# Performance work log

Hardware: AMD Instinct MI355X
Metric: run time of the kernel (lower is better)

Reference implementation:

```python
import jax, jax.numpy as jnp
import numpy as np

P = 2.0            # power-mean exponent (init kwarg p)
NUM_NODES = 1_000_000
D_FEAT = 128
NUM_GRAPHS = 4096


def setup_inputs() -> dict:
    key = jax.random.key(0)
    kx, kb = jax.random.split(key)
    x = jax.random.normal(kx, (NUM_NODES, D_FEAT), dtype=jnp.float32)
    batch = jnp.sort(jax.random.randint(kb, (NUM_NODES,), 0, NUM_GRAPHS, dtype=jnp.int64))
    return {"x": x, "batch": batch}


def reference(x, batch):
    # x: [N, D] node features; batch: [N] sorted graph ids in [0, NUM_GRAPHS)
    xp = x ** P                                                   # elementwise pow
    seg_sum = jax.ops.segment_sum(xp, batch, num_segments=NUM_GRAPHS)  # [G, D]
    counts = jax.ops.segment_sum(jnp.ones((x.shape[0],), dtype=x.dtype), batch,
                                 num_segments=NUM_GRAPHS)         # [G]
    # scatter_mean semantics: empty segments yield 0 (clamp count to avoid 0/0)
    mean = seg_sum / jnp.maximum(counts, 1.0)[:, None]            # [G, D]
    return mean ** (1.0 / P)
```

## Files before the change

### kernel.cpp

```cpp
#include <hip/hip_runtime.h>
#include <math.h>


#define D_FEAT 128
#define DV 32
#define SWEEP_GRID 2048
#define CHUNK 64

typedef float f32x4 __attribute__((ext_vector_type(4)));

__device__ __forceinline__ void nt_load4x(
    const f32x4* p0, const f32x4* p1, const f32x4* p2, const f32x4* p3,
    f32x4& v0, f32x4& v1, f32x4& v2, f32x4& v3)
{
    asm volatile(
        "global_load_dwordx4 %0, %4, off sc0 sc1 nt\n\t"
        "global_load_dwordx4 %1, %5, off sc0 sc1 nt\n\t"
        "global_load_dwordx4 %2, %6, off sc0 sc1 nt\n\t"
        "global_load_dwordx4 %3, %7, off sc0 sc1 nt\n\t"
        "s_waitcnt vmcnt(0)"
        : "=&v"(v0), "=&v"(v1), "=&v"(v2), "=&v"(v3)
        : "v"(p0), "v"(p1), "v"(p2), "v"(p3));
}

__device__ __forceinline__ f32x4 nt_load1(const f32x4* p)
{
    f32x4 v;
    asm volatile(
        "global_load_dwordx4 %0, %1, off sc0 sc1 nt\n\t"
        "s_waitcnt vmcnt(0)"
        : "=&v"(v) : "v"(p));
    return v;
}

__global__ __launch_bounds__(256) void seg_offsets_kernel(
    const int* __restrict__ batch, int* __restrict__ off, int N, int G)
{
    int i = blockIdx.x * blockDim.x + threadIdx.x;
    if (i >= N) return;
    int cur = batch[i];
    if (i == 0) {
        for (int g = 0; g <= cur; ++g) off[g] = 0;
    } else {
        int prev = batch[i - 1];
        for (int g = prev + 1; g <= cur; ++g) off[g] = i;
    }
    if (i == N - 1) {
        for (int g = cur + 1; g <= G; ++g) off[g] = N;
    }
}

__global__ __launch_bounds__(256) void zero_out_kernel(f32x4* __restrict__ out4, int n4)
{
    int i = blockIdx.x * 256 + threadIdx.x;
    if (i < n4) out4[i] = (f32x4)0.f;
}

__global__ __launch_bounds__(256) void global_powermean_pooling_44126493999223_kernel(
    const f32x4* __restrict__ x4,
    const int*   __restrict__ batch,
    const int*   __restrict__ off,
    float*       __restrict__ out,
    int N)
{
    const int tid  = threadIdx.x;
    const int fg   = tid & 31;
    const int lane = tid >> 5;

    __shared__ f32x4 red[256];

    const int nchunks = (N + CHUNK - 1) / CHUNK;
    for (int c = blockIdx.x; c < nchunks; c += SWEEP_GRID) {
        const int rs = c * CHUNK;
        const int re = (rs + CHUNK < N) ? rs + CHUNK : N;
        int cur = rs;
        int g = batch[rs];
        while (cur < re) {
            const int ge = off[g + 1];
            const int run_end = (ge < re) ? ge : re;

            f32x4 a0 = (f32x4)0.f, a1 = (f32x4)0.f, a2 = (f32x4)0.f, a3 = (f32x4)0.f;
            int r = cur + lane;
            for (; r + 24 < run_end; r += 32) {
                const f32x4* p0 = x4 + (size_t)(r     ) * DV + fg;
                const f32x4* p1 = x4 + (size_t)(r +  8) * DV + fg;
                const f32x4* p2 = x4 + (size_t)(r + 16) * DV + fg;
                const f32x4* p3 = x4 + (size_t)(r + 24) * DV + fg;
                f32x4 v0, v1, v2, v3;
                nt_load4x(p0, p1, p2, p3, v0, v1, v2, v3);
                a0 += v0 * v0; a1 += v1 * v1; a2 += v2 * v2; a3 += v3 * v3;
            }
            for (; r < run_end; r += 8) {
                f32x4 v = nt_load1(x4 + (size_t)r * DV + fg);
                a0 += v * v;
            }
            a0 += a1; a2 += a3; a0 += a2;

            red[tid] = a0;
            __syncthreads();
            if (lane < 4) red[tid] += red[tid + 128];
            __syncthreads();
            if (lane < 2) red[tid] += red[tid + 64];
            __syncthreads();
            if (lane == 0) {
                f32x4 s = red[tid] + red[tid + 32];
                float* dst = out + (size_t)g * D_FEAT + fg * 4;
                atomicAdd(dst + 0, s[0]);
                atomicAdd(dst + 1, s[1]);
                atomicAdd(dst + 2, s[2]);
                atomicAdd(dst + 3, s[3]);
            }
            __syncthreads();
            cur = run_end;
            if (cur < re) g = batch[cur];
        }
    }
}

__global__ __launch_bounds__(128) void finalize_kernel(
    const int* __restrict__ off, float* __restrict__ out)
{
    const int g = blockIdx.x;
    const int d = threadIdx.x;
    const int cnt = off[g + 1] - off[g];
    const size_t i = (size_t)g * D_FEAT + d;
    const float v = out[i];
    out[i] = (cnt > 0) ? sqrtf(v / (float)cnt) : 0.f;
}

extern "C" void kernel_launch(void* const* d_in, const int* in_sizes, int n_in,
                              void* d_out, int out_size, void* d_ws, size_t ws_size,
                              hipStream_t stream) {
    const float* x     = (const float*)d_in[0];
    const int*   batch = (const int*)d_in[1];
    float*       out   = (float*)d_out;

    const int N = in_sizes[1];
    const int G = out_size / D_FEAT;

    int* off = (int*)d_ws;

    const int n4 = G * DV;

    seg_offsets_kernel<<<(N + 255) / 256, 256, 0, stream>>>(batch, off, N, G);
    zero_out_kernel<<<(n4 + 255) / 256, 256, 0, stream>>>((f32x4*)out, n4);
    global_powermean_pooling_44126493999223_kernel
        <<<SWEEP_GRID, 256, 0, stream>>>((const f32x4*)x, batch, off, out, N);
    finalize_kernel<<<G, 128, 0, stream>>>(off, out);
}
```

Measured before the change: 637.3 us.

## Fuse zeroing and finalize into neighbouring kernels via last-contributor completion counters

```diff
diff --git a/kernel.cpp b/kernel.cpp
--- a/kernel.cpp
+++ b/kernel.cpp
@@ -5,7 +5,8 @@
 #define D_FEAT 128
 #define DV 32
 #define SWEEP_GRID 2048
-#define CHUNK 64
+#define CHUNK 128
+#define CHUNK_SHIFT 7
 
 typedef float f32x4 __attribute__((ext_vector_type(4)));
 
@@ -33,16 +34,19 @@
     return v;
 }
 
-__global__ __launch_bounds__(256) void seg_offsets_kernel(
-    const int* __restrict__ batch, int* __restrict__ off, int N, int G)
+__global__ __launch_bounds__(256) void prologue_kernel(
+    const int* __restrict__ batch, int* __restrict__ off,
+    f32x4* __restrict__ out4, int* __restrict__ contrib, int N, int G)
 {
-    int i = blockIdx.x * blockDim.x + threadIdx.x;
+    const int i = blockIdx.x * 256 + threadIdx.x;
+    if (i < G * DV) out4[i] = (f32x4)0.f;
+    if (i < G)      contrib[i] = 0;
     if (i >= N) return;
-    int cur = batch[i];
+    const int cur = batch[i];
     if (i == 0) {
         for (int g = 0; g <= cur; ++g) off[g] = 0;
     } else {
-        int prev = batch[i - 1];
+        const int prev = batch[i - 1];
         for (int g = prev + 1; g <= cur; ++g) off[g] = i;
     }
     if (i == N - 1) {
@@ -50,16 +54,11 @@
     }
 }
 
-__global__ __launch_bounds__(256) void zero_out_kernel(f32x4* __restrict__ out4, int n4)
-{
-    int i = blockIdx.x * 256 + threadIdx.x;
-    if (i < n4) out4[i] = (f32x4)0.f;
-}
-
 __global__ __launch_bounds__(256) void global_powermean_pooling_44126493999223_kernel(
     const f32x4* __restrict__ x4,
     const int*   __restrict__ batch,
     const int*   __restrict__ off,
+    int*         __restrict__ contrib,
     float*       __restrict__ out,
     int N)
 {
@@ -68,9 +67,11 @@
     const int lane = tid >> 5;
 
     __shared__ f32x4 red[256];
+    __shared__ int s_fin, s_cnt;
 
     const int nchunks = (N + CHUNK - 1) / CHUNK;
-    for (int c = blockIdx.x; c < nchunks; c += SWEEP_GRID) {
+    const int c0 = blockIdx.x + ((nchunks - 1 - blockIdx.x) / SWEEP_GRID) * SWEEP_GRID;
+    for (int c = c0; c >= 0; c -= SWEEP_GRID) {
         const int rs = c * CHUNK;
         const int re = (rs + CHUNK < N) ? rs + CHUNK : N;
         int cur = rs;
@@ -109,23 +110,30 @@
                 atomicAdd(dst + 1, s[1]);
                 atomicAdd(dst + 2, s[2]);
                 atomicAdd(dst + 3, s[3]);
+                __threadfence();
+            }
+            __syncthreads();
+            if (tid == 0) {
+                const int gs    = off[g];
+                const int total = ((ge - 1) >> CHUNK_SHIFT) - (gs >> CHUNK_SHIFT) + 1;
+                const int old   = atomicAdd(&contrib[g], 1);
+                s_fin = (old == total - 1) ? g : -1;
+                s_cnt = ge - gs;
+            }
+            __syncthreads();
+            if (s_fin >= 0) {
+                if (tid < D_FEAT) {
+                    __threadfence();
+                    float* p = out + (size_t)s_fin * D_FEAT + tid;
+                    const float v = atomicAdd(p, 0.0f);
+                    *p = sqrtf(v / (float)s_cnt);
+                }
             }
             __syncthreads();
             cur = run_end;
             if (cur < re) g = batch[cur];
         }
     }
-}
-
-__global__ __launch_bounds__(128) void finalize_kernel(
-    const int* __restrict__ off, float* __restrict__ out)
-{
-    const int g = blockIdx.x;
-    const int d = threadIdx.x;
-    const int cnt = off[g + 1] - off[g];
-    const size_t i = (size_t)g * D_FEAT + d;
-    const float v = out[i];
-    out[i] = (cnt > 0) ? sqrtf(v / (float)cnt) : 0.f;
 }
 
 extern "C" void kernel_launch(void* const* d_in, const int* in_sizes, int n_in,
@@ -138,13 +146,11 @@
     const int N = in_sizes[1];
     const int G = out_size / D_FEAT;
 
-    int* off = (int*)d_ws;
+    int* off     = (int*)d_ws;
+    int* contrib = (int*)((char*)d_ws + (64 << 10));
 
-    const int n4 = G * DV;
-
-    seg_offsets_kernel<<<(N + 255) / 256, 256, 0, stream>>>(batch, off, N, G);
-    zero_out_kernel<<<(n4 + 255) / 256, 256, 0, stream>>>((f32x4*)out, n4);
+    prologue_kernel<<<(N + 255) / 256, 256, 0, stream>>>(
+        batch, off, (f32x4*)out, contrib, N, G);
     global_powermean_pooling_44126493999223_kernel
-        <<<SWEEP_GRID, 256, 0, stream>>>((const f32x4*)x, batch, off, out, N);
-    finalize_kernel<<<G, 128, 0, stream>>>(off, out);
+        <<<SWEEP_GRID, 256, 0, stream>>>((const f32x4*)x, batch, off, contrib, out, N);
 }
```

Result: slower. 1.615 ms (+153.4%).
